# Kernel tuning notes

Measured on AMD Instinct MI355X. Metric: run time of the kernel, lower is better.

Reference implementation:

```python
import jax, jax.numpy as jnp
import numpy as np

# Dimensions
NT, NS = 1000, 2048   # timesteps, basins
NF, NG = 6, 32        # forcing channels, static attributes
NH, NR, HS = 16, 8, 256  # buckets, routing taps, hidden size
NK, NGD = 3, 9        # len(kDict)=3 (km,ki,ke), len(gDict)=9


def setup_inputs() -> dict:
    key = jax.random.key(0)
    ks = jax.random.split(key, 16)
    # Physically plausible forcings: Prcp/Evp nonnegative, T1<=T2 (min/max temp)
    Prcp = jax.random.uniform(ks[0], (NT, NS)) * 10.0
    Evp = jax.random.uniform(ks[1], (NT, NS)) * 5.0
    Tm = jax.random.normal(ks[2], (NT, NS)) * 10.0
    T1 = Tm - jax.random.uniform(ks[3], (NT, NS)) * 5.0
    T2 = Tm + jax.random.uniform(ks[4], (NT, NS)) * 5.0
    Rad = jax.random.uniform(ks[5], (NT, NS))
    Hum = jax.random.uniform(ks[6], (NT, NS))
    x = jnp.stack([Prcp, Evp, T1, T2, Rad, Hum], axis=-1)  # [nt, ns, 6]
    xc = jax.random.normal(ks[7], (NS, NG))

    def lin(k, fan_in, fan_out, s=0.05):
        k1, k2 = jax.random.split(k)
        return (jax.random.normal(k1, (fan_in, fan_out)) * s,
                jax.random.normal(k2, (fan_out,)) * s)

    W_fc, b_fc = lin(ks[8], NG, HS)
    W_r, b_r = lin(ks[9], HS, NH * (NR + 1))
    W_g, b_g = lin(ks[10], HS, NH * NGD)
    W_kin, b_kin = lin(ks[11], 4, HS)
    W_kout, b_kout = lin(ks[12], HS, NH * NK)
    return dict(x=x, xc=xc, W_fc=W_fc, b_fc=b_fc, W_r=W_r, b_r=b_r,
                W_g=W_g, b_g=b_g, W_kin=W_kin, b_kin=b_kin,
                W_kout=W_kout, b_kout=b_kout)


def _hardsigmoid(v):
    return jnp.clip(v / 6.0 + 0.5, 0.0, 1.0)


def _forward(x, xc, W_fc, b_fc, W_r, b_r, W_g, b_g, W_kin, b_kin, W_kout, b_kout):
    nt, ns, _ = x.shape
    Prcp, Evp, T1, T2 = x[..., 0], x[..., 1], x[..., 2], x[..., 3]
    f = x[..., 2:]                        # [nt, ns, 4] (T1,T2,Rad,Hum)

    # ---- getParam (eval mode: DropMask is identity) ----
    state = xc @ W_fc + b_fc              # [ns, hs]
    pK = jnp.tanh(f @ W_kin + b_kin + state) @ W_kout + b_kout  # [nt, ns, nh*3]
    hG = jnp.tanh(state)
    pG = hG @ W_g + b_g                   # [ns, nh*9]
    pR = hG @ W_r + b_r                   # [ns, nh*(nr+1)]

    # sepParam(K): km=exp, ki=relu, ke=exp  -> time-varying [nt, ns, nh]
    km = jnp.exp(pK[..., 0 * NH:1 * NH])
    ki = jax.nn.relu(pK[..., 1 * NH:2 * NH])
    ke = jnp.exp(pK[..., 2 * NH:3 * NH])

    # sepParam(G): static [ns, nh]
    g = lambda i: pG[..., i * NH:(i + 1) * NH]
    kp = jax.nn.sigmoid(g(0))
    ks_ = jax.nn.sigmoid(g(1))
    kd = jax.nn.sigmoid(g(2))
    gd = jax.nn.sigmoid(g(3))
    gl = (jax.nn.sigmoid(g(4)) * 10.0) ** 3
    qb = jax.nn.relu(g(5)) / 10.0
    ga = jax.nn.softmax(g(6), axis=-1)    # area weights over buckets
    gi = _hardsigmoid(g(7)) / 2.0
    ge = jax.nn.relu(g(8))

    # onePeakWeight: unimodal routing weights [ns, nh, nr]
    r = pR.reshape(ns, NH, NR + 1)
    s = jax.nn.softmax(r, axis=-1)
    c = jnp.cumsum(s, axis=-1)
    w = jnp.minimum(c, 1.0 - c + s)[..., :NR]
    wr = w / jnp.sum(w, axis=-1, keepdims=True)

    # divideP: snow/liquid split from min/max temperature crossing 0 C
    fl = jnp.clip(T2 / (T2 - T1 + 1e-5), 0.0, 1.0)  # liquid fraction
    Pl = (Prcp * fl)[..., None]           # [nt, ns, 1]
    Ps = (Prcp * (1.0 - fl))[..., None]
    Ev = Evp[..., None]

    # ---- bucket.step recurrence over time (the custom-scan hot loop) ----
    def step(carry, inp):
        Sf, Ss, Sg = carry                # each [ns, nh]
        Ps_t, Pl_t, Ev_t, km_t, ki_t, ke_t = inp
        # snow bucket: accumulate, melt capped by degree-day factor km
        Sf = Sf + Ps_t
        qf = jnp.minimum(Sf, km_t)
        Sf = Sf - qf
        # partition inflow: impervious/direct fraction gi
        inflow = qf + Pl_t
        qd = inflow * gi
        Ss = Ss + inflow * (1.0 - gi)
        # evapotranspiration
        E = jnp.minimum(jnp.maximum(Ss, 0.0), Ev_t * ke_t * ge)
        Ss = Ss - E
        # interflow capped by ki
        qi = jnp.minimum(ki_t, jnp.maximum(Ss, 0.0))
        Ss = Ss - qi
        # quick flow above capacity gl, slow drainage below
        qp = kp * jnp.maximum(Ss - gl, 0.0)
        qsa = ks_ * jnp.clip(Ss, 0.0, gl)
        Ss = Ss - qp - qsa
        # deep/groundwater bucket: fraction gd percolates, linear reservoir kd + baseflow qb
        Sg = Sg + qsa * gd
        qg = kd * Sg + qb
        Sg = Sg * (1.0 - kd)
        q = qp + qsa * (1.0 - gd) + qg + qd + qi
        return (Sf, Ss, Sg), q

    init = (jnp.zeros((ns, NH), x.dtype),
            jnp.zeros((ns, NH), x.dtype),
            jnp.zeros((ns, NH), x.dtype))
    _, Qp = jax.lax.scan(step, init, (Ps, Pl, Ev, km, ki, ke))  # [nt, ns, nh]

    # routing: valid temporal convolution with per-bucket unit hydrograph wr
    Tout = nt - NR + 1
    Q = jnp.zeros((Tout, ns, NH), Qp.dtype)
    for rr in range(NR):  # NR is a small fixed constant
        Q = Q + Qp[NR - 1 - rr: nt - rr] * wr[..., rr]
    yOut = jnp.sum(Q * ga, axis=-1)       # [Tout, ns]
    return yOut


def reference(x, xc, W_fc, b_fc, W_r, b_r, W_g, b_g, W_kin, b_kin, W_kout, b_kout):
    return _forward(x, xc, W_fc, b_fc, W_r, b_r, W_g, b_g, W_kin, b_kin, W_kout, b_kout)
```

## Files before the change

kernel.cpp:

```cpp
#include <hip/hip_runtime.h>
#include <hip/hip_bf16.h>

#define NT   1000
#define NS   2048
#define NH   16
#define NR   8
#define HS   256
#define TOUT 993

typedef __attribute__((ext_vector_type(8))) short short8;
typedef __attribute__((ext_vector_type(4))) float f32x4;

__device__ __forceinline__ ushort f2bf(float f) {
    union { float f; unsigned int u; } v; v.f = f;
    unsigned int u = v.u;
    return (ushort)((u + 0x7fffu + ((u >> 16) & 1u)) >> 16);
}
__device__ __forceinline__ float bf2f(ushort u) {
    union { unsigned int i; float f; } v; v.i = ((unsigned int)u) << 16; return v.f;
}
__device__ __forceinline__ unsigned int packbf2(float lo, float hi) {
    union { __hip_bfloat162 b; unsigned int u; } v;
    v.b = __float22bfloat162_rn(make_float2(lo, hi));
    return v.u;
}
__device__ __forceinline__ float sigf(float x) { return 1.f / (1.f + __expf(-x)); }
__device__ __forceinline__ float fast_tanh(float z) {
    float e = exp2f(z * 2.885390082f);
    return 1.f - 2.f * __builtin_amdgcn_rcpf(e + 1.f);
}
__device__ __forceinline__ float2 f2fma(float s, float2 w, float2 acc) {
    return make_float2(fmaf(s, w.x, acc.x), fmaf(s, w.y, acc.y));
}
template<int CTRL>
__device__ __forceinline__ float dpp_add(float v) {
    int s = __builtin_amdgcn_update_dpp(0, __builtin_bit_cast(int, v), CTRL, 0xf, 0xf, true);
    return v + __builtin_bit_cast(float, s);
}

__global__ __launch_bounds__(256) void kA(
    const float* __restrict__ xc, const float* __restrict__ W_fc, const float* __restrict__ b_fc,
    const float* __restrict__ W_r, const float* __restrict__ b_r,
    const float* __restrict__ W_g, const float* __restrict__ b_g,
    const float* __restrict__ b_kin, const float* __restrict__ W_kout,
    float* __restrict__ stateK, float* __restrict__ params, ushort* __restrict__ Wt_g)
{
    __shared__ float xcs[32];
    __shared__ float hG[256];
    __shared__ float pGR[288];
    const int s = blockIdx.x, tid = threadIdx.x;

    if (tid < 32) xcs[tid] = xc[s * 32 + tid];
    __syncthreads();

    float acc = b_fc[tid];
#pragma unroll 8
    for (int k = 0; k < 32; ++k) acc = fmaf(xcs[k], W_fc[k * 256 + tid], acc);
    stateK[s * 256 + tid] = acc + b_kin[tid];
    hG[tid] = tanhf(acc);
    __syncthreads();

    for (int j = tid; j < 288; j += 256) {
        const float* W = (j < 144) ? W_g : W_r;
        const float* b = (j < 144) ? b_g : b_r;
        int col = (j < 144) ? j : (j - 144);
        float a = b[col];
#pragma unroll 4
        for (int k = 0; k < 256; ++k) a = fmaf(hG[k], W[k * 144 + col], a);
        pGR[j] = a;
    }
    __syncthreads();

    if (tid < 16) {
        const int h = tid;
        float g0 = pGR[h],       g1 = pGR[16 + h],  g2 = pGR[32 + h];
        float g3 = pGR[48 + h],  g4 = pGR[64 + h],  g5 = pGR[80 + h];
        float g6 = pGR[96 + h],  g7 = pGR[112 + h], g8 = pGR[128 + h];
        float kp = sigf(g0), ksg = sigf(g1), kd = sigf(g2), gd = sigf(g3);
        float t4 = sigf(g4) * 10.f; float gl = t4 * t4 * t4;
        float qb = fmaxf(g5, 0.f) * 0.1f;
        float gi = fminf(fmaxf(g7 * (1.f / 6.f) + 0.5f, 0.f), 1.f) * 0.5f;
        float ge = fmaxf(g8, 0.f);
        float m = g6;
        for (int o = 1; o < 16; o <<= 1) m = fmaxf(m, __shfl_xor(m, o));
        float e = __expf(g6 - m), esum = e;
        for (int o = 1; o < 16; o <<= 1) esum += __shfl_xor(esum, o);
        float ga = e / esum;
        float r[9], rm = -1e30f;
#pragma unroll
        for (int i = 0; i < 9; ++i) { r[i] = pGR[144 + h * 9 + i]; rm = fmaxf(rm, r[i]); }
        float er[9], es = 0.f;
#pragma unroll
        for (int i = 0; i < 9; ++i) { er[i] = __expf(r[i] - rm); es += er[i]; }
        float inv_es = 1.f / es, c = 0.f, wsum = 0.f, w[8];
#pragma unroll
        for (int i = 0; i < 8; ++i) {
            float si = er[i] * inv_es; c += si;
            float wi = fminf(c, 1.f - c + si);
            w[i] = wi; wsum += wi;
        }
        const int base = s * 16 + h;
        params[0 * 32768 + base] = kp;  params[1 * 32768 + base] = ksg;
        params[2 * 32768 + base] = kd;  params[3 * 32768 + base] = gd;
        params[4 * 32768 + base] = gl;  params[5 * 32768 + base] = qb;
        params[6 * 32768 + base] = gi;  params[7 * 32768 + base] = ge;
        float sc = ga / wsum;
#pragma unroll
        for (int i = 0; i < 8; ++i) params[(8 + i) * 32768 + base] = w[i] * sc;
    }

    if (s == 0) {
        for (int i = tid; i < 48 * 256; i += 256) {
            int k = i / 48, col = i - k * 48;
            Wt_g[col * 264 + k] = f2bf(W_kout[i]);
        }
    }
}

__global__ __launch_bounds__(256, 3) void kB(
    const float* __restrict__ x,
    const float* __restrict__ stateK, const float* __restrict__ W_kin, const float* __restrict__ b_kout,
    const ushort* __restrict__ Wt_g,
    unsigned int* __restrict__ kmki, ushort* __restrict__ keA,
    float2* __restrict__ pspl, float* __restrict__ evA)
{
    __shared__ ushort Wt[48 * 264];
    __shared__ float  stS[16 * 260];
    __shared__ float  wkS[1024];
    const int tid = threadIdx.x;
    const int st = blockIdx.x & 127;
    const int tg = blockIdx.x >> 7;
    const int s0 = st << 4;

    for (int i = tid; i < 3168; i += 256)
        ((uint2*)Wt)[i] = ((const uint2*)Wt_g)[i];
#pragma unroll
    for (int i = tid; i < 1024; i += 256) {
        int row = i >> 6, c = (i & 63) << 2;
        *(float4*)(stS + row * 260 + c) = *(const float4*)(stateK + (s0 + row) * 256 + c);
    }
    *(float4*)(wkS + tid * 4) = ((const float4*)W_kin)[tid];
    __syncthreads();

    const int wv = tid >> 6, lane = tid & 63;
    const int mi = lane & 15, quad = lane >> 4;
    const int site = s0 + mi;
    const int t0 = tg * 20 + wv * 5;

    float xf[5][4];
#pragma unroll
    for (int ti = 0; ti < 5; ++ti) {
        const int t = t0 + ti;
        const int xb = (t * 2048 + site) * 6;
        float2 u23 = *(const float2*)(x + xb + 2);
        float2 u45 = *(const float2*)(x + xb + 4);
        xf[ti][0] = u23.x; xf[ti][1] = u23.y; xf[ti][2] = u45.x; xf[ti][3] = u45.y;
        if (lane < 16) {
            float2 u01 = *(const float2*)(x + xb);
            float fl = fminf(fmaxf(u23.y * __builtin_amdgcn_rcpf(u23.y - u23.x + 1e-5f), 0.f), 1.f);
            const int sg = st * 4 + (mi >> 2), sl = mi & 3;
            const int mo = (sg * 1000 + t) * 4 + sl;
            pspl[mo] = make_float2(u01.x * (1.f - fl), u01.x * fl);
            evA[mo]  = u01.y;
        }
    }

    const float* stp = stS + mi * 260 + quad * 8;
    const float* wkp = wkS + quad * 8;
    const ushort* Wt0 = Wt + mi * 264 + quad * 8;

    f32x4 acc[5][3];
#pragma unroll
    for (int ti = 0; ti < 5; ++ti)
#pragma unroll
        for (int j = 0; j < 3; ++j) acc[ti][j] = (f32x4){0.f, 0.f, 0.f, 0.f};

#pragma unroll 1
    for (int kk = 0; kk < 8; ++kk) {
        const int ko = kk * 32;
        float4 sa  = *(const float4*)(stp + ko);
        float4 sb  = *(const float4*)(stp + ko + 4);
        float4 w0a = *(const float4*)(wkp + ko);
        float4 w0b = *(const float4*)(wkp + ko + 4);
        float4 w1a = *(const float4*)(wkp + 256 + ko);
        float4 w1b = *(const float4*)(wkp + 256 + ko + 4);
        float4 w2a = *(const float4*)(wkp + 512 + ko);
        float4 w2b = *(const float4*)(wkp + 512 + ko + 4);
        float4 w3a = *(const float4*)(wkp + 768 + ko);
        float4 w3b = *(const float4*)(wkp + 768 + ko + 4);
        short8 b0 = *(const short8*)(Wt0 + ko);
        short8 b1 = *(const short8*)(Wt0 + 16 * 264 + ko);
        short8 b2 = *(const short8*)(Wt0 + 32 * 264 + ko);
#pragma unroll
        for (int ti = 0; ti < 5; ++ti) {
            const float x0 = xf[ti][0], x1 = xf[ti][1], x2 = xf[ti][2], x3 = xf[ti][3];
            float2 z0 = make_float2(sa.x, sa.y), z1 = make_float2(sa.z, sa.w);
            float2 z2 = make_float2(sb.x, sb.y), z3 = make_float2(sb.z, sb.w);
            z0 = f2fma(x0, make_float2(w0a.x, w0a.y), z0);
            z1 = f2fma(x0, make_float2(w0a.z, w0a.w), z1);
            z2 = f2fma(x0, make_float2(w0b.x, w0b.y), z2);
            z3 = f2fma(x0, make_float2(w0b.z, w0b.w), z3);
            z0 = f2fma(x1, make_float2(w1a.x, w1a.y), z0);
            z1 = f2fma(x1, make_float2(w1a.z, w1a.w), z1);
            z2 = f2fma(x1, make_float2(w1b.x, w1b.y), z2);
            z3 = f2fma(x1, make_float2(w1b.z, w1b.w), z3);
            z0 = f2fma(x2, make_float2(w2a.x, w2a.y), z0);
            z1 = f2fma(x2, make_float2(w2a.z, w2a.w), z1);
            z2 = f2fma(x2, make_float2(w2b.x, w2b.y), z2);
            z3 = f2fma(x2, make_float2(w2b.z, w2b.w), z3);
            z0 = f2fma(x3, make_float2(w3a.x, w3a.y), z0);
            z1 = f2fma(x3, make_float2(w3a.z, w3a.w), z1);
            z2 = f2fma(x3, make_float2(w3b.x, w3b.y), z2);
            z3 = f2fma(x3, make_float2(w3b.z, w3b.w), z3);
            union { short8 s; unsigned int u[4]; } a;
            a.u[0] = packbf2(fast_tanh(z0.x), fast_tanh(z0.y));
            a.u[1] = packbf2(fast_tanh(z1.x), fast_tanh(z1.y));
            a.u[2] = packbf2(fast_tanh(z2.x), fast_tanh(z2.y));
            a.u[3] = packbf2(fast_tanh(z3.x), fast_tanh(z3.y));
            acc[ti][0] = __builtin_amdgcn_mfma_f32_16x16x32_bf16(a.s, b0, acc[ti][0], 0, 0, 0);
            acc[ti][1] = __builtin_amdgcn_mfma_f32_16x16x32_bf16(a.s, b1, acc[ti][1], 0, 0, 0);
            acc[ti][2] = __builtin_amdgcn_mfma_f32_16x16x32_bf16(a.s, b2, acc[ti][2], 0, 0, 0);
        }
    }

    const float bo0 = b_kout[mi], bo1 = b_kout[16 + mi], bo2 = b_kout[32 + mi];
    const int sgW = st * 4 + quad;
#pragma unroll
    for (int ti = 0; ti < 5; ++ti) {
        const int t = t0 + ti;
#pragma unroll
        for (int reg = 0; reg < 4; ++reg) {
            float km = __expf(acc[ti][0][reg] + bo0);
            float ki = fmaxf(acc[ti][1][reg] + bo1, 0.f);
            float ke = __expf(acc[ti][2][reg] + bo2);
            const int idx = (sgW * 1000 + t) * 64 + (reg << 4) + mi;
            kmki[idx] = (unsigned int)f2bf(km) | ((unsigned int)f2bf(ki) << 16);
            keA[idx]  = f2bf(ke);
        }
    }
}

__global__ __launch_bounds__(64, 1) void kC(
    const unsigned int* __restrict__ kmki, const ushort* __restrict__ keA,
    const float2* __restrict__ pspl, const float* __restrict__ evA,
    const float* __restrict__ params, float* __restrict__ yOut)
{
    const int tid = threadIdx.x;
    const int sg = blockIdx.x;
    const int s = sg * 4 + (tid >> 4);
    const int h = tid & 15;
    const int gid = s * 16 + h;
    const int sl = tid >> 4;

    const float kp  = params[0 * 32768 + gid];
    const float ksg = params[1 * 32768 + gid];
    const float kd  = params[2 * 32768 + gid];
    const float gd  = params[3 * 32768 + gid];
    const float gl  = params[4 * 32768 + gid];
    const float qbv = params[5 * 32768 + gid];
    const float gi  = params[6 * 32768 + gid];
    const float ge  = params[7 * 32768 + gid];
    float wrga[8];
#pragma unroll
    for (int i = 0; i < 8; ++i) wrga[i] = params[(8 + i) * 32768 + gid];

    float Sf = 0.f, Ss = 0.f, Sg = 0.f;
    float qh[8];
#pragma unroll
    for (int i = 0; i < 8; ++i) qh[i] = 0.f;

    const int base = sg * 1000;

    unsigned int a0[8], a1[8]; ushort e0[8], e1[8];
    float2 p0[8], p1[8]; float v0[8], v1[8];

#define LOADB(B, tb) do {                                               \
        const int _b = base + (tb) * 8;                                 \
        _Pragma("unroll")                                               \
        for (int i = 0; i < 8; ++i) {                                   \
            a##B[i] = kmki[(_b + i) * 64 + tid];                        \
            e##B[i] = keA[(_b + i) * 64 + tid];                         \
            p##B[i] = pspl[(_b + i) * 4 + sl];                          \
            v##B[i] = evA[(_b + i) * 4 + sl];                           \
        }                                                               \
    } while (0)

#define COMPUTEB(B, tb) do {                                            \
        float z[8];                                                     \
        _Pragma("unroll")                                               \
        for (int i = 0; i < 8; ++i) {                                   \
            float km = bf2f((ushort)(a##B[i] & 0xffffu));               \
            float ki = bf2f((ushort)(a##B[i] >> 16));                   \
            float ke = bf2f(e##B[i]);                                   \
            float ps = p##B[i].x, pl = p##B[i].y, ev = v##B[i];         \
            Sf += ps;                                                   \
            float qf = fminf(Sf, km); Sf -= qf;                         \
            float inflow = qf + pl;                                     \
            float qd = inflow * gi;                                     \
            Ss += inflow * (1.f - gi);                                  \
            float E = fminf(fmaxf(Ss, 0.f), ev * ke * ge); Ss -= E;     \
            float qi = fminf(ki, fmaxf(Ss, 0.f)); Ss -= qi;             \
            float qp = kp * fmaxf(Ss - gl, 0.f);                        \
            float qsa = ksg * fminf(fmaxf(Ss, 0.f), gl);                \
            Ss -= qp + qsa;                                             \
            Sg += qsa * gd;                                             \
            float qg = kd * Sg + qbv;                                   \
            Sg *= (1.f - kd);                                           \
            float q = qp + qsa * (1.f - gd) + qg + qd + qi;             \
            qh[i] = q;                                                  \
            float v = 0.f;                                              \
            _Pragma("unroll")                                           \
            for (int k = 0; k < 8; ++k) v = fmaf(wrga[k], qh[(i - k) & 7], v); \
            z[i] = v;                                                   \
        }                                                               \
        _Pragma("unroll")                                               \
        for (int i = 0; i < 8; ++i) z[i] = dpp_add<0xB1>(z[i]);    \
        _Pragma("unroll")                                               \
        for (int i = 0; i < 8; ++i) z[i] = dpp_add<0x4E>(z[i]);    \
        _Pragma("unroll")                                               \
        for (int i = 0; i < 8; ++i) z[i] = dpp_add<0x141>(z[i]);   \
        _Pragma("unroll")                                               \
        for (int i = 0; i < 8; ++i) z[i] = dpp_add<0x140>(z[i]);   \
        if (h == 0) {                                                   \
            const int tbase = (tb) * 8;                                 \
            _Pragma("unroll")                                           \
            for (int i = 0; i < 8; ++i) {                               \
                const int t = tbase + i;                                \
                if (t >= 7) yOut[(t - 7) * 2048 + s] = z[i];            \
            }                                                           \
        }                                                               \
    } while (0)

    LOADB(0, 0);
    LOADB(1, 1);

    for (int tb2 = 0; tb2 < 63; ++tb2) {
        const int tbA = 2 * tb2;
        COMPUTEB(0, tbA);
        {
            const int pf = (tbA + 2 < 125) ? tbA + 2 : 124;
            LOADB(0, pf);
        }
        const int tbB = 2 * tb2 + 1;
        if (tbB < 125) {
            COMPUTEB(1, tbB);
            const int pf = (tbB + 2 < 125) ? tbB + 2 : 124;
            LOADB(1, pf);
        }
    }
#undef LOADB
#undef COMPUTEB
}

extern "C" void kernel_launch(void* const* d_in, const int* in_sizes, int n_in,
                              void* d_out, int out_size, void* d_ws, size_t ws_size,
                              hipStream_t stream) {
    const float* x      = (const float*)d_in[0];
    const float* xc     = (const float*)d_in[1];
    const float* W_fc   = (const float*)d_in[2];
    const float* b_fc   = (const float*)d_in[3];
    const float* W_r    = (const float*)d_in[4];
    const float* b_r    = (const float*)d_in[5];
    const float* W_g    = (const float*)d_in[6];
    const float* b_g    = (const float*)d_in[7];
    const float* W_kin  = (const float*)d_in[8];
    const float* b_kin  = (const float*)d_in[9];
    const float* W_kout = (const float*)d_in[10];
    const float* b_kout = (const float*)d_in[11];
    float* yOut = (float*)d_out;

    char* ws = (char*)d_ws;
    float*  stateK = (float*)(ws + 0);
    float*  params = (float*)(ws + (2 << 20));
    ushort* Wt_g   = (ushort*)(ws + (4 << 20));
    char*   p      = ws + (4 << 20) + (128 << 10);
    float2* pspl   = (float2*)p;
    float*  evA    = (float*)(p + 16384000);
    unsigned int* kmki = (unsigned int*)(p + 16384000 + 8192000);
    ushort* keA    = (ushort*)(p + 16384000 + 8192000 + 131072000);

    hipLaunchKernelGGL(kA, dim3(2048), dim3(256), 0, stream,
                       xc, W_fc, b_fc, W_r, b_r, W_g, b_g, b_kin, W_kout,
                       stateK, params, Wt_g);
    hipLaunchKernelGGL(kB, dim3(128 * 50), dim3(256), 0, stream,
                       x, stateK, W_kin, b_kout, Wt_g, kmki, keA, pspl, evA);
    hipLaunchKernelGGL(kC, dim3(512), dim3(64), 0, stream,
                       kmki, keA, pspl, evA, params, yOut);
}
```

Baseline: 577.5 us.

## Fold evaporation product into kB and triple-buffer the kC scan

kB now computes ev*ke*ge per timestep and bucket and stores it as one bf16 stream. That removes the separate evA array and its loads inside kC's sequential recurrence. kA precomputes 1-gi, 1-kd and 1-gd, and kC's step drops several clamps to zero (relying on storage staying nonnegative) and uses fma forms. The kC prefetch moves from double to triple buffering to hide more load latency. In exchange, the evaporation cap is rounded to bf16 as a product, and kC holds more registers for the extra buffer.

Result: faster. 560.9 us (-2.9%).

```diff
diff --git a/kernel.cpp b/kernel.cpp
--- a/kernel.cpp
+++ b/kernel.cpp
@@ -100,13 +100,15 @@
             w[i] = wi; wsum += wi;
         }
         const int base = s * 16 + h;
-        params[0 * 32768 + base] = kp;  params[1 * 32768 + base] = ksg;
-        params[2 * 32768 + base] = kd;  params[3 * 32768 + base] = gd;
-        params[4 * 32768 + base] = gl;  params[5 * 32768 + base] = qb;
-        params[6 * 32768 + base] = gi;  params[7 * 32768 + base] = ge;
+        params[0 * 32768 + base] = kp;       params[1 * 32768 + base] = ksg;
+        params[2 * 32768 + base] = kd;       params[3 * 32768 + base] = gd;
+        params[4 * 32768 + base] = gl;       params[5 * 32768 + base] = qb;
+        params[6 * 32768 + base] = gi;       params[7 * 32768 + base] = 1.f - gi;
+        params[8 * 32768 + base] = 1.f - kd; params[9 * 32768 + base] = 1.f - gd;
+        params[10 * 32768 + base] = ge;
         float sc = ga / wsum;
 #pragma unroll
-        for (int i = 0; i < 8; ++i) params[(8 + i) * 32768 + base] = w[i] * sc;
+        for (int i = 0; i < 8; ++i) params[(11 + i) * 32768 + base] = w[i] * sc;
     }
 
     if (s == 0) {
@@ -120,13 +122,15 @@
 __global__ __launch_bounds__(256, 3) void kB(
     const float* __restrict__ x,
     const float* __restrict__ stateK, const float* __restrict__ W_kin, const float* __restrict__ b_kout,
-    const ushort* __restrict__ Wt_g,
-    unsigned int* __restrict__ kmki, ushort* __restrict__ keA,
-    float2* __restrict__ pspl, float* __restrict__ evA)
+    const ushort* __restrict__ Wt_g, const float* __restrict__ params,
+    unsigned int* __restrict__ kmki, ushort* __restrict__ kevA,
+    float2* __restrict__ pspl)
 {
     __shared__ ushort Wt[48 * 264];
     __shared__ float  stS[16 * 260];
     __shared__ float  wkS[1024];
+    __shared__ float  geS[256];
+    __shared__ float  evS[4][5][16];
     const int tid = threadIdx.x;
     const int st = blockIdx.x & 127;
     const int tg = blockIdx.x >> 7;
@@ -140,6 +144,7 @@
         *(float4*)(stS + row * 260 + c) = *(const float4*)(stateK + (s0 + row) * 256 + c);
     }
     *(float4*)(wkS + tid * 4) = ((const float4*)W_kin)[tid];
+    geS[tid] = params[10 * 32768 + s0 * 16 + tid];
     __syncthreads();
 
     const int wv = tid >> 6, lane = tid & 63;
@@ -159,9 +164,8 @@
             float2 u01 = *(const float2*)(x + xb);
             float fl = fminf(fmaxf(u23.y * __builtin_amdgcn_rcpf(u23.y - u23.x + 1e-5f), 0.f), 1.f);
             const int sg = st * 4 + (mi >> 2), sl = mi & 3;
-            const int mo = (sg * 1000 + t) * 4 + sl;
-            pspl[mo] = make_float2(u01.x * (1.f - fl), u01.x * fl);
-            evA[mo]  = u01.y;
+            pspl[(sg * 1000 + t) * 4 + sl] = make_float2(u01.x * (1.f - fl), u01.x * fl);
+            evS[wv][ti][mi] = u01.y;
         }
     }
 
@@ -230,39 +234,43 @@
         const int t = t0 + ti;
 #pragma unroll
         for (int reg = 0; reg < 4; ++reg) {
+            const int sl = quad * 4 + reg;
             float km = __expf(acc[ti][0][reg] + bo0);
             float ki = fmaxf(acc[ti][1][reg] + bo1, 0.f);
             float ke = __expf(acc[ti][2][reg] + bo2);
+            float kev = ke * evS[wv][ti][sl] * geS[sl * 16 + mi];
             const int idx = (sgW * 1000 + t) * 64 + (reg << 4) + mi;
             kmki[idx] = (unsigned int)f2bf(km) | ((unsigned int)f2bf(ki) << 16);
-            keA[idx]  = f2bf(ke);
+            kevA[idx] = f2bf(kev);
         }
     }
 }
 
 __global__ __launch_bounds__(64, 1) void kC(
-    const unsigned int* __restrict__ kmki, const ushort* __restrict__ keA,
-    const float2* __restrict__ pspl, const float* __restrict__ evA,
+    const unsigned int* __restrict__ kmki, const ushort* __restrict__ kevA,
+    const float2* __restrict__ pspl,
     const float* __restrict__ params, float* __restrict__ yOut)
 {
     const int tid = threadIdx.x;
     const int sg = blockIdx.x;
-    const int s = sg * 4 + (tid >> 4);
+    const int sl = tid >> 4;
+    const int s = sg * 4 + sl;
     const int h = tid & 15;
     const int gid = s * 16 + h;
-    const int sl = tid >> 4;
 
     const float kp  = params[0 * 32768 + gid];
-    const float ksg = params[1 * 32768 + gid];
+    const float ks_ = params[1 * 32768 + gid];
     const float kd  = params[2 * 32768 + gid];
     const float gd  = params[3 * 32768 + gid];
     const float gl  = params[4 * 32768 + gid];
     const float qbv = params[5 * 32768 + gid];
     const float gi  = params[6 * 32768 + gid];
-    const float ge  = params[7 * 32768 + gid];
+    const float gi1 = params[7 * 32768 + gid];
+    const float kd1 = params[8 * 32768 + gid];
+    const float gd1 = params[9 * 32768 + gid];
     float wrga[8];
 #pragma unroll
-    for (int i = 0; i < 8; ++i) wrga[i] = params[(8 + i) * 32768 + gid];
+    for (int i = 0; i < 8; ++i) wrga[i] = params[(11 + i) * 32768 + gid];
 
     float Sf = 0.f, Ss = 0.f, Sg = 0.f;
     float qh[8];
@@ -271,17 +279,16 @@
 
     const int base = sg * 1000;
 
-    unsigned int a0[8], a1[8]; ushort e0[8], e1[8];
-    float2 p0[8], p1[8]; float v0[8], v1[8];
+    unsigned int a0[8], a1[8], a2[8]; ushort e0[8], e1[8], e2[8];
+    float2 p0[8], p1[8], p2[8];
 
 #define LOADB(B, tb) do {                                               \
         const int _b = base + (tb) * 8;                                 \
         _Pragma("unroll")                                               \
         for (int i = 0; i < 8; ++i) {                                   \
             a##B[i] = kmki[(_b + i) * 64 + tid];                        \
-            e##B[i] = keA[(_b + i) * 64 + tid];                         \
+            e##B[i] = kevA[(_b + i) * 64 + tid];                        \
             p##B[i] = pspl[(_b + i) * 4 + sl];                          \
-            v##B[i] = evA[(_b + i) * 4 + sl];                           \
         }                                                               \
     } while (0)
 
@@ -289,24 +296,24 @@
         float z[8];                                                     \
         _Pragma("unroll")                                               \
         for (int i = 0; i < 8; ++i) {                                   \
-            float km = bf2f((ushort)(a##B[i] & 0xffffu));               \
-            float ki = bf2f((ushort)(a##B[i] >> 16));                   \
-            float ke = bf2f(e##B[i]);                                   \
-            float ps = p##B[i].x, pl = p##B[i].y, ev = v##B[i];         \
+            float km = __builtin_bit_cast(float, a##B[i] << 16);        \
+            float ki = __builtin_bit_cast(float, a##B[i] & 0xffff0000u);\
+            float kev = __builtin_bit_cast(float, ((unsigned int)e##B[i]) << 16); \
+            float ps = p##B[i].x, pl = p##B[i].y;                       \
             Sf += ps;                                                   \
             float qf = fminf(Sf, km); Sf -= qf;                         \
             float inflow = qf + pl;                                     \
             float qd = inflow * gi;                                     \
-            Ss += inflow * (1.f - gi);                                  \
-            float E = fminf(fmaxf(Ss, 0.f), ev * ke * ge); Ss -= E;     \
-            float qi = fminf(ki, fmaxf(Ss, 0.f)); Ss -= qi;             \
+            Ss = fmaf(inflow, gi1, Ss);                                 \
+            float E = fminf(Ss, kev); Ss -= E;                          \
+            float qi = fminf(ki, Ss); Ss -= qi;                         \
             float qp = kp * fmaxf(Ss - gl, 0.f);                        \
-            float qsa = ksg * fminf(fmaxf(Ss, 0.f), gl);                \
+            float qsa = ks_ * fminf(Ss, gl);                            \
             Ss -= qp + qsa;                                             \
-            Sg += qsa * gd;                                             \
-            float qg = kd * Sg + qbv;                                   \
-            Sg *= (1.f - kd);                                           \
-            float q = qp + qsa * (1.f - gd) + qg + qd + qi;             \
+            Sg = fmaf(qsa, gd, Sg);                                     \
+            float qg = fmaf(kd, Sg, qbv);                               \
+            Sg *= kd1;                                                  \
+            float q = fmaf(qsa, gd1, qp) + qg + qd + qi;                \
             qh[i] = q;                                                  \
             float v = 0.f;                                              \
             _Pragma("unroll")                                           \
@@ -314,13 +321,13 @@
             z[i] = v;                                                   \
         }                                                               \
         _Pragma("unroll")                                               \
-        for (int i = 0; i < 8; ++i) z[i] = dpp_add<0xB1>(z[i]);    \
-        _Pragma("unroll")                                               \
-        for (int i = 0; i < 8; ++i) z[i] = dpp_add<0x4E>(z[i]);    \
-        _Pragma("unroll")                                               \
-        for (int i = 0; i < 8; ++i) z[i] = dpp_add<0x141>(z[i]);   \
-        _Pragma("unroll")                                               \
-        for (int i = 0; i < 8; ++i) z[i] = dpp_add<0x140>(z[i]);   \
+        for (int i = 0; i < 8; ++i) z[i] = dpp_add<0xB1>(z[i]);         \
+        _Pragma("unroll")                                               \
+        for (int i = 0; i < 8; ++i) z[i] = dpp_add<0x4E>(z[i]);         \
+        _Pragma("unroll")                                               \
+        for (int i = 0; i < 8; ++i) z[i] = dpp_add<0x141>(z[i]);        \
+        _Pragma("unroll")                                               \
+        for (int i = 0; i < 8; ++i) z[i] = dpp_add<0x140>(z[i]);        \
         if (h == 0) {                                                   \
             const int tbase = (tb) * 8;                                 \
             _Pragma("unroll")                                           \
@@ -333,19 +340,19 @@
 
     LOADB(0, 0);
     LOADB(1, 1);
-
-    for (int tb2 = 0; tb2 < 63; ++tb2) {
-        const int tbA = 2 * tb2;
-        COMPUTEB(0, tbA);
-        {
-            const int pf = (tbA + 2 < 125) ? tbA + 2 : 124;
-            LOADB(0, pf);
-        }
-        const int tbB = 2 * tb2 + 1;
-        if (tbB < 125) {
-            COMPUTEB(1, tbB);
-            const int pf = (tbB + 2 < 125) ? tbB + 2 : 124;
-            LOADB(1, pf);
+    LOADB(2, 2);
+
+    for (int it = 0; it < 42; ++it) {
+        const int tb = it * 3;
+        COMPUTEB(0, tb);
+        LOADB(0, (tb + 3 <= 124) ? tb + 3 : 124);
+        if (tb + 1 < 125) {
+            COMPUTEB(1, tb + 1);
+            LOADB(1, (tb + 4 <= 124) ? tb + 4 : 124);
+        }
+        if (tb + 2 < 125) {
+            COMPUTEB(2, tb + 2);
+            LOADB(2, (tb + 5 <= 124) ? tb + 5 : 124);
         }
     }
 #undef LOADB
@@ -372,18 +379,17 @@
     char* ws = (char*)d_ws;
     float*  stateK = (float*)(ws + 0);
     float*  params = (float*)(ws + (2 << 20));
-    ushort* Wt_g   = (ushort*)(ws + (4 << 20));
-    char*   p      = ws + (4 << 20) + (128 << 10);
+    ushort* Wt_g   = (ushort*)(ws + (6 << 20));
+    char*   p      = ws + (6 << 20) + (128 << 10);
     float2* pspl   = (float2*)p;
-    float*  evA    = (float*)(p + 16384000);
-    unsigned int* kmki = (unsigned int*)(p + 16384000 + 8192000);
-    ushort* keA    = (ushort*)(p + 16384000 + 8192000 + 131072000);
+    unsigned int* kmki = (unsigned int*)(p + 16384000);
+    ushort* kevA   = (ushort*)(p + 16384000 + 131072000);
 
     hipLaunchKernelGGL(kA, dim3(2048), dim3(256), 0, stream,
                        xc, W_fc, b_fc, W_r, b_r, W_g, b_g, b_kin, W_kout,
                        stateK, params, Wt_g);
     hipLaunchKernelGGL(kB, dim3(128 * 50), dim3(256), 0, stream,
-                       x, stateK, W_kin, b_kout, Wt_g, kmki, keA, pspl, evA);
+                       x, stateK, W_kin, b_kout, Wt_g, params, kmki, kevA, pspl);
     hipLaunchKernelGGL(kC, dim3(512), dim3(64), 0, stream,
-                       kmki, keA, pspl, evA, params, yOut);
-}
+                       kmki, kevA, pspl, params, yOut);
+}
```
